# Kernel optimization log

Measured on AMD Instinct MI355X. Metric: run time of the kernel, lower is better.

The kernel has to match this reference:

```python
import jax, jax.numpy as jnp
import numpy as np
import math

D_MODEL = 1024
N_HEADS = 16
D_HEAD = D_MODEL // N_HEADS
B, S = 4, 2048


def setup_inputs() -> dict:
    key = jax.random.key(0)
    ks = jax.random.split(key, 9)
    std = 1.0 / math.sqrt(D_MODEL)
    x = jax.random.normal(ks[0], (B, S, D_MODEL), dtype=jnp.float32)
    # causal mask: True = masked out
    mask = jnp.triu(jnp.ones((S, S), dtype=bool), k=1)
    Wq = jax.random.normal(ks[1], (D_MODEL, D_MODEL), jnp.float32) * std
    bq = jnp.zeros((D_MODEL,), jnp.float32)
    Wk = jax.random.normal(ks[2], (D_MODEL, D_MODEL), jnp.float32) * std
    bk = jnp.zeros((D_MODEL,), jnp.float32)
    Wv = jax.random.normal(ks[3], (D_MODEL, D_MODEL), jnp.float32) * std
    bv = jnp.zeros((D_MODEL,), jnp.float32)
    Wo = jax.random.normal(ks[4], (D_MODEL, D_MODEL), jnp.float32) * std
    bo = jnp.zeros((D_MODEL,), jnp.float32)
    return {"x": x, "mask": mask, "Wq": Wq, "bq": bq, "Wk": Wk, "bk": bk,
            "Wv": Wv, "bv": bv, "Wo": Wo, "bo": bo}


def reference(x, mask, Wq, bq, Wk, bk, Wv, bv, Wo, bo):
    b, s, _ = x.shape
    scale = math.sqrt(D_HEAD)
    # projections (Linear: x @ W.T + b), reshape to [b, h, s, d]
    def proj(W, bias):
        y = jnp.einsum('bsd,ed->bse', x, W) + bias
        return y.reshape(b, s, N_HEADS, D_HEAD).transpose(0, 2, 1, 3)
    q = proj(Wq, bq)
    k = proj(Wk, bk)
    v = proj(Wv, bv)
    scores = jnp.einsum('bhqd,bhkd->bhqk', q, k) / scale  # [b,h,s,s]
    scores = jnp.where(mask[None, None, :, :], -jnp.inf, scores)
    attn = jax.nn.softmax(scores, axis=-1)
    # dropout is identity in eval mode
    out = jnp.einsum('bhqk,bhkd->bhqd', attn, v)
    out = out.transpose(0, 2, 1, 3).reshape(b, s, D_MODEL)
    return jnp.einsum('bsd,ed->bse', out, Wo) + bo
```

## Files before the change

### kernel.cpp

```cpp
#include <hip/hip_runtime.h>
#include <stdint.h>

#define NH 16
#define DH 64
#define DM 1024
#define Bz 4
#define Sz 2048
#define NKT 16

typedef __bf16 bf16x8 __attribute__((ext_vector_type(8)));
typedef float f32x4 __attribute__((ext_vector_type(4)));
typedef float f32x16 __attribute__((ext_vector_type(16)));

#define GLD_LDS16(gsrc, ldst)                                             \
    __builtin_amdgcn_global_load_lds(                                     \
        (const __attribute__((address_space(1))) void*)(gsrc),            \
        (__attribute__((address_space(3))) void*)(ldst), 16, 0, 0)

__device__ __forceinline__ unsigned short f2bf(float f) {
    unsigned u = __float_as_uint(f);
    u += 0x7FFFu + ((u >> 16) & 1u);
    return (unsigned short)(u >> 16);
}
__device__ __forceinline__ float bf2f(unsigned short h) {
    return __uint_as_float(((unsigned)h) << 16);
}

__global__ void detect_dtype(const unsigned short* __restrict__ xs,
                             int* __restrict__ flagp)
{
    const int t = threadIdx.x;
    int cnt = 0;
    for (int i = 0; i < 64; i++) {
        const unsigned short h = xs[(t * 64 + i) * 2];
        const int e = (h >> 7) & 0xFF;
        if (h != 0 && e >= 100 && e <= 130) cnt++;
    }
#pragma unroll
    for (int off = 32; off >= 1; off >>= 1)
        cnt += __shfl_xor(cnt, off);
    if (t == 0) *flagp = (cnt < 2048) ? 1 : 0;
}

__global__ __launch_bounds__(256) void convert_inputs(
    const void* s0, const void* s1, const void* s2, const void* s3,
    const void* s4, const void* s5, const void* s6, const void* s7,
    const void* s8,
    unsigned short* d0, unsigned short* d1, unsigned short* d2,
    unsigned short* d3, unsigned short* d4, unsigned short* d5,
    unsigned short* d6, unsigned short* d7, unsigned short* d8,
    const int* __restrict__ flagp)
{
    const void* s; unsigned short* d; int n;
    switch (blockIdx.y) {
        case 0: s = s0; d = d0; n = Bz * Sz * DM; break;
        case 1: s = s1; d = d1; n = DM * DM; break;
        case 2: s = s2; d = d2; n = DM * DM; break;
        case 3: s = s3; d = d3; n = DM * DM; break;
        case 4: s = s4; d = d4; n = DM * DM; break;
        case 5: s = s5; d = d5; n = DM; break;
        case 6: s = s6; d = d6; n = DM; break;
        case 7: s = s7; d = d7; n = DM; break;
        default: s = s8; d = d8; n = DM; break;
    }
    const int flag   = *flagp;
    const int stride = gridDim.x * blockDim.x * 4;
    const int base   = (blockIdx.x * blockDim.x + threadIdx.x) * 4;
    if (flag) {
        const float* sf = (const float*)s;
        for (int i = base; i < n; i += stride) {
            const float4 v = *reinterpret_cast<const float4*>(&sf[i]);
            ushort2 a, b;
            a.x = f2bf(v.x); a.y = f2bf(v.y);
            b.x = f2bf(v.z); b.y = f2bf(v.w);
            *reinterpret_cast<ushort2*>(&d[i])     = a;
            *reinterpret_cast<ushort2*>(&d[i + 2]) = b;
        }
    } else {
        const unsigned short* sh = (const unsigned short*)s;
        for (int i = base; i < n; i += stride)
            *reinterpret_cast<uint2*>(&d[i]) = *reinterpret_cast<const uint2*>(&sh[i]);
    }
}


__global__ __launch_bounds__(256, 2) void gemm_qkv(
    const unsigned short* __restrict__ X,
    const unsigned short* __restrict__ Wq,
    const unsigned short* __restrict__ Wk,
    const unsigned short* __restrict__ Wv,
    const unsigned short* __restrict__ bq,
    const unsigned short* __restrict__ bk,
    const unsigned short* __restrict__ bv,
    unsigned short* __restrict__ Qb,
    unsigned short* __restrict__ Kb,
    unsigned short* __restrict__ Vtb)
{
    __shared__ __align__(16) unsigned short As[2][128 * 64];
    __shared__ __align__(16) unsigned short Bs[2][128 * 64];

    const int tid  = threadIdx.x;
    const int w    = tid >> 6, lane = tid & 63;
    const int l31  = lane & 31, half = lane >> 5;
    const int wm   = (w & 1) * 64, wn = (w >> 1) * 64;

    const int flat = (int)(blockIdx.y * gridDim.x + blockIdx.x);
    const int k8   = flat & 7;
    const int m    = flat >> 3;
    const int proj = m >> 6;
    const int mm   = m & 63;
    const int bm   = (k8 * 8 + (mm >> 3)) * 128;
    const int bn   = (mm & 7) * 128;

    const unsigned short* W      = proj == 0 ? Wq : (proj == 1 ? Wk : Wv);
    const unsigned short* bias_p = proj == 0 ? bq : (proj == 1 ? bk : bv);
    const unsigned short* Abase  = X + (size_t)bm * DM;
    const unsigned short* Bbase  = W + (size_t)bn * DM;

    const int sr8 = lane >> 3;
    const int sce = ((lane & 7) ^ sr8) * 8;

    f32x16 acc[2][2];
#pragma unroll
    for (int i = 0; i < 2; i++)
#pragma unroll
        for (int j = 0; j < 2; j++)
#pragma unroll
            for (int e = 0; e < 16; e++)
                acc[i][j][e] = 0.f;

    auto stage = [&](int buf, int kt) {
        const int kc = kt * 64;
#pragma unroll
        for (int t = 0; t < 4; t++) {
            const int r = w * 32 + t * 8;
            GLD_LDS16(&Abase[(size_t)(r + sr8) * DM + kc + sce], &As[buf][r * 64]);
            GLD_LDS16(&Bbase[(size_t)(r + sr8) * DM + kc + sce], &Bs[buf][r * 64]);
        }
    };

    auto frg = [&](const unsigned short* base, int row, int cb) {
        const int cs = cb ^ ((row & 7) << 4);
        return *reinterpret_cast<const bf16x8*>(
            reinterpret_cast<const char*>(base) + row * 128 + cs);
    };

    stage(0, 0);
    asm volatile("s_waitcnt vmcnt(0)" ::: "memory");
    __builtin_amdgcn_s_barrier();
    asm volatile("" ::: "memory");

    for (int T = 0; T < NKT; ++T) {
        if (T < NKT - 1) stage((T + 1) & 1, T + 1);
        const unsigned short* A = &As[T & 1][0];
        const unsigned short* B = &Bs[T & 1][0];
#pragma unroll
        for (int s = 0; s < 4; s++) {
            const int cb = s * 32 + half * 16;
            const bf16x8 a0 = frg(A, wm + l31,      cb);
            const bf16x8 a1 = frg(A, wm + 32 + l31, cb);
            const bf16x8 b0 = frg(B, wn + l31,      cb);
            const bf16x8 b1 = frg(B, wn + 32 + l31, cb);
            acc[0][0] = __builtin_amdgcn_mfma_f32_32x32x16_bf16(a0, b0, acc[0][0], 0, 0, 0);
            acc[0][1] = __builtin_amdgcn_mfma_f32_32x32x16_bf16(a0, b1, acc[0][1], 0, 0, 0);
            acc[1][0] = __builtin_amdgcn_mfma_f32_32x32x16_bf16(a1, b0, acc[1][0], 0, 0, 0);
            acc[1][1] = __builtin_amdgcn_mfma_f32_32x32x16_bf16(a1, b1, acc[1][1], 0, 0, 0);
        }
        asm volatile("s_waitcnt vmcnt(0)" ::: "memory");
        __builtin_amdgcn_s_barrier();
        asm volatile("" ::: "memory");
    }

    if (proj < 2) {
        unsigned short* dst = (proj == 0) ? Qb : Kb;
#pragma unroll
        for (int nj = 0; nj < 2; nj++) {
            const int   e    = bn + wn + nj * 32 + l31;
            const int   h    = e >> 6, dd = e & 63;
            const float bias = bf2f(bias_p[e]);
#pragma unroll
            for (int mi = 0; mi < 2; mi++) {
#pragma unroll
                for (int reg = 0; reg < 16; reg++) {
                    const int mrow = bm + wm + mi * 32 + (reg & 3) + 8 * (reg >> 2) + 4 * half;
                    const int b = mrow >> 11, s = mrow & 2047;
                    dst[((size_t)(b * NH + h) * Sz + s) * DH + dd] = f2bf(acc[mi][nj][reg] + bias);
                }
            }
        }
    } else {
#pragma unroll
        for (int nj = 0; nj < 2; nj++) {
            const int   e    = bn + wn + nj * 32 + l31;
            const int   h    = e >> 6, dd = e & 63;
            const float bias = bf2f(bias_p[e]);
#pragma unroll
            for (int mi = 0; mi < 2; mi++) {
#pragma unroll
                for (int g = 0; g < 4; g++) {
                    const int m0 = bm + wm + mi * 32 + 8 * g + 4 * half;
                    const int b  = m0 >> 11, s0 = m0 & 2047;
                    const unsigned u0 = __float_as_uint(acc[mi][nj][4 * g + 0] + bias) + 0x8000u;
                    const unsigned u1 = __float_as_uint(acc[mi][nj][4 * g + 1] + bias) + 0x8000u;
                    const unsigned u2 = __float_as_uint(acc[mi][nj][4 * g + 2] + bias) + 0x8000u;
                    const unsigned u3 = __float_as_uint(acc[mi][nj][4 * g + 3] + bias) + 0x8000u;
                    uint2 pk;
                    pk.x = __builtin_amdgcn_perm(u1, u0, 0x07060302u);
                    pk.y = __builtin_amdgcn_perm(u3, u2, 0x07060302u);
                    *reinterpret_cast<uint2*>(
                        &Vtb[((size_t)(b * NH + h) * DH + dd) * Sz + s0]) = pk;
                }
            }
        }
    }
}

__global__ __launch_bounds__(512) void flash_attn(
    const unsigned short* __restrict__ Qb,
    const unsigned short* __restrict__ Kb,
    const unsigned short* __restrict__ Vtb,
    unsigned short* __restrict__ AOb)
{
    __shared__ __align__(16) unsigned short Ks[64 * 72];
    __shared__ __align__(16) unsigned short Vs[64 * 72];
    __shared__ __align__(16) unsigned short Ps[128 * 72];

    const int tid  = threadIdx.x;
    const int w    = tid >> 6, lane = tid & 63;
    const int quad = lane >> 4, l15 = lane & 15;

    const int flat = (int)(blockIdx.y * gridDim.x + blockIdx.x);
    const int k8   = flat & 7;
    const int m    = flat >> 3;
    const int bh   = k8 + 8 * (m >> 3);
    const int cA   = m & 7;

    const int srow = tid >> 3;
    const int scc  = (tid & 7) * 8;
    const int hh = bh & 15, bb = bh >> 4;

    for (int pass = 0; pass < 2; pass++) {
        const int chunk = pass ? (15 - cA) : cA;
        const int qb = chunk * 128;
        const int qw = qb + w * 16;

        const size_t qbase = ((size_t)bh * Sz + qw + l15) * DH;
        const bf16x8 qf0 = *reinterpret_cast<const bf16x8*>(&Qb[qbase + quad * 8]);
        const bf16x8 qf1 = *reinterpret_cast<const bf16x8*>(&Qb[qbase + 32 + quad * 8]);

        f32x4 o[4];
#pragma unroll
        for (int jd = 0; jd < 4; jd++) o[jd] = f32x4{0.f, 0.f, 0.f, 0.f};
        float lsum = 0.f;

        const int n_kv = qb + 128;

        auto compute = [&](int kb) {
            const bool need_mask = (kb + 64 > qw);
#pragma unroll
            for (int j = 0; j < 4; j++) {
                const bf16x8 kf0 = *reinterpret_cast<const bf16x8*>(&Ks[(j * 16 + l15) * 72 + quad * 8]);
                const bf16x8 kf1 = *reinterpret_cast<const bf16x8*>(&Ks[(j * 16 + l15) * 72 + 32 + quad * 8]);
                f32x4 st = f32x4{0.f, 0.f, 0.f, 0.f};
                st = __builtin_amdgcn_mfma_f32_16x16x32_bf16(kf0, qf0, st, 0, 0, 0);
                st = __builtin_amdgcn_mfma_f32_16x16x32_bf16(kf1, qf1, st, 0, 0, 0);
                const int qa = qw + l15;
                float p[4];
#pragma unroll
                for (int r = 0; r < 4; r++) {
                    float e = __builtin_amdgcn_exp2f(st[r] * 0.18033688011f);
                    if (need_mask) {
                        const int kv = kb + j * 16 + quad * 4 + r;
                        e = (kv <= qa) ? e : 0.f;
                    }
                    p[r] = e;
                }
                lsum += (p[0] + p[1]) + (p[2] + p[3]);
                const unsigned u0 = __float_as_uint(p[0]) + 0x8000u;
                const unsigned u1 = __float_as_uint(p[1]) + 0x8000u;
                const unsigned u2 = __float_as_uint(p[2]) + 0x8000u;
                const unsigned u3 = __float_as_uint(p[3]) + 0x8000u;
                const unsigned pk0 = __builtin_amdgcn_perm(u1, u0, 0x07060302u);
                const unsigned pk1 = __builtin_amdgcn_perm(u3, u2, 0x07060302u);
                const int prow = (w * 16 + l15) * 72 + j * 16 + quad * 4;
                *reinterpret_cast<unsigned*>(&Ps[prow])     = pk0;
                *reinterpret_cast<unsigned*>(&Ps[prow + 2]) = pk1;
            }

            asm volatile("s_waitcnt lgkmcnt(0)" ::: "memory");

            const bf16x8 pf0 = *reinterpret_cast<const bf16x8*>(&Ps[(w * 16 + l15) * 72 + quad * 8]);
            const bf16x8 pf1 = *reinterpret_cast<const bf16x8*>(&Ps[(w * 16 + l15) * 72 + 32 + quad * 8]);
#pragma unroll
            for (int jd = 0; jd < 4; jd++) {
                const bf16x8 vf0 = *reinterpret_cast<const bf16x8*>(&Vs[(jd * 16 + l15) * 72 + quad * 8]);
                const bf16x8 vf1 = *reinterpret_cast<const bf16x8*>(&Vs[(jd * 16 + l15) * 72 + 32 + quad * 8]);
                o[jd] = __builtin_amdgcn_mfma_f32_16x16x32_bf16(pf0, vf0, o[jd], 0, 0, 0);
                o[jd] = __builtin_amdgcn_mfma_f32_16x16x32_bf16(pf1, vf1, o[jd], 0, 0, 0);
            }
        };

        uint4 kr0 = *reinterpret_cast<const uint4*>(&Kb[((size_t)bh * Sz + srow) * DH + scc]);
        uint4 vr0 = *reinterpret_cast<const uint4*>(&Vtb[((size_t)bh * DH + srow) * Sz + scc]);
        uint4 kr1, vr1;

        for (int kb = 0; kb < n_kv; kb += 128) {
            __syncthreads();
            *reinterpret_cast<uint4*>(&Ks[srow * 72 + scc]) = kr0;
            *reinterpret_cast<uint4*>(&Vs[srow * 72 + scc]) = vr0;
            kr1 = *reinterpret_cast<const uint4*>(&Kb[((size_t)bh * Sz + kb + 64 + srow) * DH + scc]);
            vr1 = *reinterpret_cast<const uint4*>(&Vtb[((size_t)bh * DH + srow) * Sz + kb + 64 + scc]);
            asm volatile("s_waitcnt lgkmcnt(0)" ::: "memory");
            __builtin_amdgcn_s_barrier();
            asm volatile("" ::: "memory");
            if (kb <= qw + 15) compute(kb);

            __syncthreads();
            *reinterpret_cast<uint4*>(&Ks[srow * 72 + scc]) = kr1;
            *reinterpret_cast<uint4*>(&Vs[srow * 72 + scc]) = vr1;
            if (kb + 128 < n_kv) {
                kr0 = *reinterpret_cast<const uint4*>(&Kb[((size_t)bh * Sz + kb + 128 + srow) * DH + scc]);
                vr0 = *reinterpret_cast<const uint4*>(&Vtb[((size_t)bh * DH + srow) * Sz + kb + 128 + scc]);
            }
            asm volatile("s_waitcnt lgkmcnt(0)" ::: "memory");
            __builtin_amdgcn_s_barrier();
            asm volatile("" ::: "memory");
            if (kb + 64 <= qw + 15) compute(kb + 64);
        }

        lsum += __shfl_xor(lsum, 16);
        lsum += __shfl_xor(lsum, 32);

        float linv[4];
#pragma unroll
        for (int r = 0; r < 4; r++)
            linv[r] = 1.0f / __shfl(lsum, quad * 4 + r);
#pragma unroll
        for (int jd = 0; jd < 4; jd++) {
#pragma unroll
            for (int r = 0; r < 4; r++) {
                const int s = qw + quad * 4 + r;
                AOb[((size_t)(bb * Sz + s)) * DM + hh * DH + jd * 16 + l15] =
                    f2bf(o[jd][r] * linv[r]);
            }
        }
    }
}

__global__ __launch_bounds__(256, 2) void gemm_out(
    const unsigned short* __restrict__ Ain,
    const unsigned short* __restrict__ W,
    const unsigned short* __restrict__ bo,
    void* __restrict__ outv,
    const int* __restrict__ flagp)
{
    __shared__ __align__(16) unsigned short As[2][128 * 64];
    __shared__ __align__(16) unsigned short Bs[2][128 * 64];

    const int tid  = threadIdx.x;
    const int w    = tid >> 6, lane = tid & 63;
    const int l31  = lane & 31, half = lane >> 5;
    const int wm   = (w & 1) * 64, wn = (w >> 1) * 64;

    const int flat = (int)(blockIdx.y * gridDim.x + blockIdx.x);
    const int k8   = flat & 7;
    const int m    = flat >> 3;
    const int bm   = (k8 * 8 + (m >> 3)) * 128;
    const int bn   = (m & 7) * 128;

    const unsigned short* Abase = Ain + (size_t)bm * DM;
    const unsigned short* Bbase = W   + (size_t)bn * DM;

    const int sr8 = lane >> 3;
    const int sce = ((lane & 7) ^ sr8) * 8;

    f32x16 acc[2][2];
#pragma unroll
    for (int i = 0; i < 2; i++)
#pragma unroll
        for (int j = 0; j < 2; j++)
#pragma unroll
            for (int e = 0; e < 16; e++)
                acc[i][j][e] = 0.f;

    auto stage = [&](int buf, int kt) {
        const int kc = kt * 64;
#pragma unroll
        for (int t = 0; t < 4; t++) {
            const int r = w * 32 + t * 8;
            GLD_LDS16(&Abase[(size_t)(r + sr8) * DM + kc + sce], &As[buf][r * 64]);
            GLD_LDS16(&Bbase[(size_t)(r + sr8) * DM + kc + sce], &Bs[buf][r * 64]);
        }
    };

    auto frg = [&](const unsigned short* base, int row, int cb) {
        const int cs = cb ^ ((row & 7) << 4);
        return *reinterpret_cast<const bf16x8*>(
            reinterpret_cast<const char*>(base) + row * 128 + cs);
    };

    stage(0, 0);
    asm volatile("s_waitcnt vmcnt(0)" ::: "memory");
    __builtin_amdgcn_s_barrier();
    asm volatile("" ::: "memory");

    for (int T = 0; T < NKT; ++T) {
        if (T < NKT - 1) stage((T + 1) & 1, T + 1);
        const unsigned short* A = &As[T & 1][0];
        const unsigned short* B = &Bs[T & 1][0];
#pragma unroll
        for (int s = 0; s < 4; s++) {
            const int cb = s * 32 + half * 16;
            const bf16x8 a0 = frg(A, wm + l31,      cb);
            const bf16x8 a1 = frg(A, wm + 32 + l31, cb);
            const bf16x8 b0 = frg(B, wn + l31,      cb);
            const bf16x8 b1 = frg(B, wn + 32 + l31, cb);
            acc[0][0] = __builtin_amdgcn_mfma_f32_32x32x16_bf16(a0, b0, acc[0][0], 0, 0, 0);
            acc[0][1] = __builtin_amdgcn_mfma_f32_32x32x16_bf16(a0, b1, acc[0][1], 0, 0, 0);
            acc[1][0] = __builtin_amdgcn_mfma_f32_32x32x16_bf16(a1, b0, acc[1][0], 0, 0, 0);
            acc[1][1] = __builtin_amdgcn_mfma_f32_32x32x16_bf16(a1, b1, acc[1][1], 0, 0, 0);
        }
        asm volatile("s_waitcnt vmcnt(0)" ::: "memory");
        __builtin_amdgcn_s_barrier();
        asm volatile("" ::: "memory");
    }

    const int flag = *flagp;
    float*          outf = (float*)outv;
    unsigned short* outh = (unsigned short*)outv;
#pragma unroll
    for (int nj = 0; nj < 2; nj++) {
        const int   e    = bn + wn + nj * 32 + l31;
        const float bias = bf2f(bo[e]);
#pragma unroll
        for (int mi = 0; mi < 2; mi++) {
#pragma unroll
            for (int reg = 0; reg < 16; reg++) {
                const int   mrow = bm + wm + mi * 32 + (reg & 3) + 8 * (reg >> 2) + 4 * half;
                const float v = acc[mi][nj][reg] + bias;
                if (flag) outf[(size_t)mrow * DM + e] = v;
                else      outh[(size_t)mrow * DM + e] = f2bf(v);
            }
        }
    }
}

extern "C" void kernel_launch(void* const* d_in, const int* in_sizes, int n_in,
                              void* d_out, int out_size, void* d_ws, size_t ws_size,
                              hipStream_t stream) {
    const void* x = nullptr;
    const void* Wsrc[4] = {nullptr, nullptr, nullptr, nullptr};
    const void* bsrc[4] = {nullptr, nullptr, nullptr, nullptr};
    int nw = 0, nb = 0;
    for (int i = 0; i < n_in; i++) {
        const int sz = in_sizes[i];
        if (sz == Bz * Sz * DM)            { if (!x) x = d_in[i]; }
        else if (sz == DM * DM)            { if (nw < 4) Wsrc[nw++] = d_in[i]; }
        else if (sz == DM)                 { if (nb < 4) bsrc[nb++] = d_in[i]; }
    }

    char* wsb = (char*)d_ws;
    int*  flagp = (int*)wsb;
    unsigned short* Xc  = (unsigned short*)(wsb + 16);
    const size_t NX = (size_t)Bz * Sz * DM;
    const size_t NW = (size_t)DM * DM;
    unsigned short* Wc0 = Xc  + NX;
    unsigned short* Wc1 = Wc0 + NW;
    unsigned short* Wc2 = Wc1 + NW;
    unsigned short* Wc3 = Wc2 + NW;
    unsigned short* bc0 = Wc3 + NW;
    unsigned short* bc1 = bc0 + DM;
    unsigned short* bc2 = bc1 + DM;
    unsigned short* bc3 = bc2 + DM;
    unsigned short* Qb  = bc3 + DM;
    const size_t SZ = (size_t)Bz * NH * Sz * DH;
    unsigned short* Kb  = Qb  + SZ;
    unsigned short* Vtb = Kb  + SZ;
    unsigned short* AOb = Vtb + SZ;

    detect_dtype<<<1, 64, 0, stream>>>((const unsigned short*)x, flagp);
    convert_inputs<<<dim3(512, 9), 256, 0, stream>>>(
        x, Wsrc[0], Wsrc[1], Wsrc[2], Wsrc[3],
        bsrc[0], bsrc[1], bsrc[2], bsrc[3],
        Xc, Wc0, Wc1, Wc2, Wc3, bc0, bc1, bc2, bc3, flagp);

    gemm_qkv <<<dim3(24, 64), 256, 0, stream>>>(Xc, Wc0, Wc1, Wc2, bc0, bc1, bc2, Qb, Kb, Vtb);
    flash_attn<<<dim3(8, 64), 512, 0, stream>>>(Qb, Kb, Vtb, AOb);
    gemm_out <<<dim3(8, 64), 256, 0, stream>>>(AOb, Wc3, bc3, d_out, flagp);
}
```

Measured before the change: 288.3 us.

## Widen convert stores, stage 128-key tiles in flash attention, single-buffer gemm_out

The dtype-convert kernel now processes 8 elements per thread with 16-byte stores. Flash attention stages a full 128-key K/V block into shared memory per iteration, halving the number of barriers, and prefetches the next 128-key block into registers. gemm_out drops LDS double buffering in favour of a single buffer with a wait before compute, raising the occupancy hint to 4 blocks per CU. The gemm_out change loses load/compute overlap within a block and relies on extra resident blocks to hide latency.

Measured after the change: 279.4 us. 3.1% less time.

```diff
diff --git a/kernel.cpp b/kernel.cpp
--- a/kernel.cpp
+++ b/kernel.cpp
@@ -24,6 +24,9 @@
 }
 __device__ __forceinline__ float bf2f(unsigned short h) {
     return __uint_as_float(((unsigned)h) << 16);
+}
+__device__ __forceinline__ unsigned pack2bf(float a, float b) {
+    return (unsigned)f2bf(a) | ((unsigned)f2bf(b) << 16);
 }
 
 __global__ void detect_dtype(const unsigned short* __restrict__ xs,
@@ -64,22 +67,24 @@
         default: s = s8; d = d8; n = DM; break;
     }
     const int flag   = *flagp;
-    const int stride = gridDim.x * blockDim.x * 4;
-    const int base   = (blockIdx.x * blockDim.x + threadIdx.x) * 4;
+    const int stride = gridDim.x * blockDim.x * 8;
+    const int base   = (blockIdx.x * blockDim.x + threadIdx.x) * 8;
     if (flag) {
         const float* sf = (const float*)s;
         for (int i = base; i < n; i += stride) {
-            const float4 v = *reinterpret_cast<const float4*>(&sf[i]);
-            ushort2 a, b;
-            a.x = f2bf(v.x); a.y = f2bf(v.y);
-            b.x = f2bf(v.z); b.y = f2bf(v.w);
-            *reinterpret_cast<ushort2*>(&d[i])     = a;
-            *reinterpret_cast<ushort2*>(&d[i + 2]) = b;
+            const float4 v0 = *reinterpret_cast<const float4*>(&sf[i]);
+            const float4 v1 = *reinterpret_cast<const float4*>(&sf[i + 4]);
+            uint4 o;
+            o.x = pack2bf(v0.x, v0.y);
+            o.y = pack2bf(v0.z, v0.w);
+            o.z = pack2bf(v1.x, v1.y);
+            o.w = pack2bf(v1.z, v1.w);
+            *reinterpret_cast<uint4*>(&d[i]) = o;
         }
     } else {
         const unsigned short* sh = (const unsigned short*)s;
         for (int i = base; i < n; i += stride)
-            *reinterpret_cast<uint2*>(&d[i]) = *reinterpret_cast<const uint2*>(&sh[i]);
+            *reinterpret_cast<uint4*>(&d[i]) = *reinterpret_cast<const uint4*>(&sh[i]);
     }
 }
 
@@ -221,8 +226,8 @@
     const unsigned short* __restrict__ Vtb,
     unsigned short* __restrict__ AOb)
 {
-    __shared__ __align__(16) unsigned short Ks[64 * 72];
-    __shared__ __align__(16) unsigned short Vs[64 * 72];
+    __shared__ __align__(16) unsigned short Ks[128 * 72];
+    __shared__ __align__(16) unsigned short Vs[64 * 136];
     __shared__ __align__(16) unsigned short Ps[128 * 72];
 
     const int tid  = threadIdx.x;
@@ -255,12 +260,13 @@
 
         const int n_kv = qb + 128;
 
-        auto compute = [&](int kb) {
-            const bool need_mask = (kb + 64 > qw);
+        auto compute = [&](int kbe) {
+            const int  off       = kbe & 127;
+            const bool need_mask = (kbe + 64 > qw);
 #pragma unroll
             for (int j = 0; j < 4; j++) {
-                const bf16x8 kf0 = *reinterpret_cast<const bf16x8*>(&Ks[(j * 16 + l15) * 72 + quad * 8]);
-                const bf16x8 kf1 = *reinterpret_cast<const bf16x8*>(&Ks[(j * 16 + l15) * 72 + 32 + quad * 8]);
+                const bf16x8 kf0 = *reinterpret_cast<const bf16x8*>(&Ks[(off + j * 16 + l15) * 72 + quad * 8]);
+                const bf16x8 kf1 = *reinterpret_cast<const bf16x8*>(&Ks[(off + j * 16 + l15) * 72 + 32 + quad * 8]);
                 f32x4 st = f32x4{0.f, 0.f, 0.f, 0.f};
                 st = __builtin_amdgcn_mfma_f32_16x16x32_bf16(kf0, qf0, st, 0, 0, 0);
                 st = __builtin_amdgcn_mfma_f32_16x16x32_bf16(kf1, qf1, st, 0, 0, 0);
@@ -270,7 +276,7 @@
                 for (int r = 0; r < 4; r++) {
                     float e = __builtin_amdgcn_exp2f(st[r] * 0.18033688011f);
                     if (need_mask) {
-                        const int kv = kb + j * 16 + quad * 4 + r;
+                        const int kv = kbe + j * 16 + quad * 4 + r;
                         e = (kv <= qa) ? e : 0.f;
                     }
                     p[r] = e;
@@ -293,38 +299,34 @@
             const bf16x8 pf1 = *reinterpret_cast<const bf16x8*>(&Ps[(w * 16 + l15) * 72 + 32 + quad * 8]);
 #pragma unroll
             for (int jd = 0; jd < 4; jd++) {
-                const bf16x8 vf0 = *reinterpret_cast<const bf16x8*>(&Vs[(jd * 16 + l15) * 72 + quad * 8]);
-                const bf16x8 vf1 = *reinterpret_cast<const bf16x8*>(&Vs[(jd * 16 + l15) * 72 + 32 + quad * 8]);
+                const bf16x8 vf0 = *reinterpret_cast<const bf16x8*>(&Vs[(jd * 16 + l15) * 136 + off + quad * 8]);
+                const bf16x8 vf1 = *reinterpret_cast<const bf16x8*>(&Vs[(jd * 16 + l15) * 136 + off + 32 + quad * 8]);
                 o[jd] = __builtin_amdgcn_mfma_f32_16x16x32_bf16(pf0, vf0, o[jd], 0, 0, 0);
                 o[jd] = __builtin_amdgcn_mfma_f32_16x16x32_bf16(pf1, vf1, o[jd], 0, 0, 0);
             }
         };
 
         uint4 kr0 = *reinterpret_cast<const uint4*>(&Kb[((size_t)bh * Sz + srow) * DH + scc]);
+        uint4 kr1 = *reinterpret_cast<const uint4*>(&Kb[((size_t)bh * Sz + 64 + srow) * DH + scc]);
         uint4 vr0 = *reinterpret_cast<const uint4*>(&Vtb[((size_t)bh * DH + srow) * Sz + scc]);
-        uint4 kr1, vr1;
+        uint4 vr1 = *reinterpret_cast<const uint4*>(&Vtb[((size_t)bh * DH + srow) * Sz + 64 + scc]);
 
         for (int kb = 0; kb < n_kv; kb += 128) {
             __syncthreads();
-            *reinterpret_cast<uint4*>(&Ks[srow * 72 + scc]) = kr0;
-            *reinterpret_cast<uint4*>(&Vs[srow * 72 + scc]) = vr0;
-            kr1 = *reinterpret_cast<const uint4*>(&Kb[((size_t)bh * Sz + kb + 64 + srow) * DH + scc]);
-            vr1 = *reinterpret_cast<const uint4*>(&Vtb[((size_t)bh * DH + srow) * Sz + kb + 64 + scc]);
+            *reinterpret_cast<uint4*>(&Ks[srow * 72 + scc])        = kr0;
+            *reinterpret_cast<uint4*>(&Ks[(64 + srow) * 72 + scc]) = kr1;
+            *reinterpret_cast<uint4*>(&Vs[srow * 136 + scc])       = vr0;
+            *reinterpret_cast<uint4*>(&Vs[srow * 136 + 64 + scc])  = vr1;
+            if (kb + 128 < n_kv) {
+                kr0 = *reinterpret_cast<const uint4*>(&Kb[((size_t)bh * Sz + kb + 128 + srow) * DH + scc]);
+                kr1 = *reinterpret_cast<const uint4*>(&Kb[((size_t)bh * Sz + kb + 192 + srow) * DH + scc]);
+                vr0 = *reinterpret_cast<const uint4*>(&Vtb[((size_t)bh * DH + srow) * Sz + kb + 128 + scc]);
+                vr1 = *reinterpret_cast<const uint4*>(&Vtb[((size_t)bh * DH + srow) * Sz + kb + 192 + scc]);
+            }
             asm volatile("s_waitcnt lgkmcnt(0)" ::: "memory");
             __builtin_amdgcn_s_barrier();
             asm volatile("" ::: "memory");
-            if (kb <= qw + 15) compute(kb);
-
-            __syncthreads();
-            *reinterpret_cast<uint4*>(&Ks[srow * 72 + scc]) = kr1;
-            *reinterpret_cast<uint4*>(&Vs[srow * 72 + scc]) = vr1;
-            if (kb + 128 < n_kv) {
-                kr0 = *reinterpret_cast<const uint4*>(&Kb[((size_t)bh * Sz + kb + 128 + srow) * DH + scc]);
-                vr0 = *reinterpret_cast<const uint4*>(&Vtb[((size_t)bh * DH + srow) * Sz + kb + 128 + scc]);
-            }
-            asm volatile("s_waitcnt lgkmcnt(0)" ::: "memory");
-            __builtin_amdgcn_s_barrier();
-            asm volatile("" ::: "memory");
+            if (kb <= qw + 15)      compute(kb);
             if (kb + 64 <= qw + 15) compute(kb + 64);
         }
 
@@ -347,15 +349,15 @@
     }
 }
 
-__global__ __launch_bounds__(256, 2) void gemm_out(
+__global__ __launch_bounds__(256, 4) void gemm_out(
     const unsigned short* __restrict__ Ain,
     const unsigned short* __restrict__ W,
     const unsigned short* __restrict__ bo,
     void* __restrict__ outv,
     const int* __restrict__ flagp)
 {
-    __shared__ __align__(16) unsigned short As[2][128 * 64];
-    __shared__ __align__(16) unsigned short Bs[2][128 * 64];
+    __shared__ __align__(16) unsigned short As[128 * 64];
+    __shared__ __align__(16) unsigned short Bs[128 * 64];
 
     const int tid  = threadIdx.x;
     const int w    = tid >> 6, lane = tid & 63;
@@ -383,13 +385,13 @@
             for (int e = 0; e < 16; e++)
                 acc[i][j][e] = 0.f;
 
-    auto stage = [&](int buf, int kt) {
+    auto stage = [&](int kt) {
         const int kc = kt * 64;
 #pragma unroll
         for (int t = 0; t < 4; t++) {
             const int r = w * 32 + t * 8;
-            GLD_LDS16(&Abase[(size_t)(r + sr8) * DM + kc + sce], &As[buf][r * 64]);
-            GLD_LDS16(&Bbase[(size_t)(r + sr8) * DM + kc + sce], &Bs[buf][r * 64]);
+            GLD_LDS16(&Abase[(size_t)(r + sr8) * DM + kc + sce], &As[r * 64]);
+            GLD_LDS16(&Bbase[(size_t)(r + sr8) * DM + kc + sce], &Bs[r * 64]);
         }
     };
 
@@ -399,28 +401,23 @@
             reinterpret_cast<const char*>(base) + row * 128 + cs);
     };
 
-    stage(0, 0);
-    asm volatile("s_waitcnt vmcnt(0)" ::: "memory");
-    __builtin_amdgcn_s_barrier();
-    asm volatile("" ::: "memory");
-
     for (int T = 0; T < NKT; ++T) {
-        if (T < NKT - 1) stage((T + 1) & 1, T + 1);
-        const unsigned short* A = &As[T & 1][0];
-        const unsigned short* B = &Bs[T & 1][0];
+        stage(T);
+        asm volatile("s_waitcnt vmcnt(0)" ::: "memory");
+        __builtin_amdgcn_s_barrier();
+        asm volatile("" ::: "memory");
 #pragma unroll
         for (int s = 0; s < 4; s++) {
             const int cb = s * 32 + half * 16;
-            const bf16x8 a0 = frg(A, wm + l31,      cb);
-            const bf16x8 a1 = frg(A, wm + 32 + l31, cb);
-            const bf16x8 b0 = frg(B, wn + l31,      cb);
-            const bf16x8 b1 = frg(B, wn + 32 + l31, cb);
+            const bf16x8 a0 = frg(As, wm + l31,      cb);
+            const bf16x8 a1 = frg(As, wm + 32 + l31, cb);
+            const bf16x8 b0 = frg(Bs, wn + l31,      cb);
+            const bf16x8 b1 = frg(Bs, wn + 32 + l31, cb);
             acc[0][0] = __builtin_amdgcn_mfma_f32_32x32x16_bf16(a0, b0, acc[0][0], 0, 0, 0);
             acc[0][1] = __builtin_amdgcn_mfma_f32_32x32x16_bf16(a0, b1, acc[0][1], 0, 0, 0);
             acc[1][0] = __builtin_amdgcn_mfma_f32_32x32x16_bf16(a1, b0, acc[1][0], 0, 0, 0);
             acc[1][1] = __builtin_amdgcn_mfma_f32_32x32x16_bf16(a1, b1, acc[1][1], 0, 0, 0);
         }
-        asm volatile("s_waitcnt vmcnt(0)" ::: "memory");
         __builtin_amdgcn_s_barrier();
         asm volatile("" ::: "memory");
     }
```
